# Kernel optimization log

Hardware: AMD Instinct MI355X
Metric: run time of the kernel (lower is better)

Reference implementation:

```python
import jax, jax.numpy as jnp
import numpy as np

EMBED_DIM = 1024
NUM_HEADS = 16
HEAD_DIM = EMBED_DIM // NUM_HEADS
B, T = 2, 2048


def setup_inputs() -> dict:
    key = jax.random.key(0)
    ks = jax.random.split(key, 5)
    s_in = 1.0 / np.sqrt(EMBED_DIM)
    return {
        "x": jax.random.normal(ks[0], (B, T, EMBED_DIM), dtype=jnp.float32),
        "qkv_w": jax.random.uniform(ks[1], (3 * EMBED_DIM, EMBED_DIM), jnp.float32, -s_in, s_in),
        "qkv_b": jax.random.uniform(ks[2], (3 * EMBED_DIM,), jnp.float32, -s_in, s_in),
        "out_w": jax.random.uniform(ks[3], (EMBED_DIM, EMBED_DIM), jnp.float32, -s_in, s_in),
        "out_b": jax.random.uniform(ks[4], (EMBED_DIM,), jnp.float32, -s_in, s_in),
    }


def reference(x, qkv_w, qkv_b, out_w, out_b):
    b, t, d = x.shape
    scale = HEAD_DIM ** -0.5
    # fused qkv projection: (B, T, 3D)
    qkv = jnp.einsum("btd,ed->bte", x, qkv_w) + qkv_b
    qkv = qkv.reshape(b, t, 3, NUM_HEADS, HEAD_DIM)
    q, k, v = jnp.moveaxis(qkv, 2, 0)  # each (B, T, H, Dh)
    # scores: (B, H, T, T)
    scores = jnp.einsum("bqhd,bkhd->bhqk", q, k) * scale
    attn = jax.nn.softmax(scores, axis=-1)
    # attention output: (B, T, H, Dh) -> (B, T, D)
    ctx = jnp.einsum("bhqk,bkhd->bqhd", attn, v).reshape(b, t, d)
    return jnp.einsum("btd,ed->bte", ctx, out_w) + out_b
```

## Files before the change

### kernel.cpp

```cpp
#include <hip/hip_runtime.h>

typedef __bf16 bf16;
typedef __bf16 bf16x4 __attribute__((ext_vector_type(4)));
typedef __bf16 bf16x8 __attribute__((ext_vector_type(8)));
typedef float f32x4 __attribute__((ext_vector_type(4)));

#define MFMA16(a, b, c) __builtin_amdgcn_mfma_f32_16x16x32_bf16(a, b, c, 0, 0, 0)

__device__ __forceinline__ void lds_load16(void* lds, const void* g) {
  __builtin_amdgcn_global_load_lds(
      (const __attribute__((address_space(1))) unsigned int*)g,
      (__attribute__((address_space(3))) unsigned int*)lds, 16, 0, 0);
}

__global__ void cvt3(const float* __restrict__ x, const float* __restrict__ qw,
                     const float* __restrict__ ow, bf16* __restrict__ xb,
                     bf16* __restrict__ qwb, bf16* __restrict__ owb) {
  const int i = blockIdx.x * blockDim.x + threadIdx.x;
  const float* src;
  bf16* dst;
  int k;
  if (i < 1048576) {
    src = x; dst = xb; k = i;
  } else if (i < 1048576 + 786432) {
    src = qw; dst = qwb; k = i - 1048576;
  } else {
    src = ow; dst = owb; k = i - (1048576 + 786432);
  }
  const float4 v = ((const float4*)src)[k];
  bf16x4 o;
  o[0] = (bf16)v.x; o[1] = (bf16)v.y; o[2] = (bf16)v.z; o[3] = (bf16)v.w;
  ((bf16x4*)dst)[k] = o;
}

template <int MODE>
__global__ __launch_bounds__(256, 2) void gemm_bt(
    const bf16* __restrict__ A, const bf16* __restrict__ B,
    const float* __restrict__ bias, float* __restrict__ Cf,
    bf16* __restrict__ Qb, bf16* __restrict__ Kb, bf16* __restrict__ VT,
    int N, int K) {
  __shared__ bf16 As[128][64];
  __shared__ bf16 Bs[128][64];
  const int tid = threadIdx.x;
  const int w = tid >> 6, lane = tid & 63;
  const int l15 = lane & 15, quad = lane >> 4;
  const int lr = lane >> 3;
  const int lc = (lane & 7) * 8;
  const int bn = blockIdx.x, bm = blockIdx.y;
  const int wm = (w >> 1) * 64, wn = (w & 1) * 64;

  const bf16* Abase = A + (size_t)(bm * 128) * K;
  const bf16* Bbase = B + (size_t)(bn * 128) * K;

  f32x4 acc[4][4] = {};

  for (int k0 = 0; k0 < K; k0 += 64) {
#pragma unroll
    for (int c = 0; c < 4; ++c) {
      const int row = w * 32 + c * 8;
      lds_load16(&As[row][0], Abase + (size_t)(row + lr) * K + k0 + lc);
      lds_load16(&Bs[row][0], Bbase + (size_t)(row + lr) * K + k0 + lc);
    }
    __syncthreads();
#pragma unroll
    for (int kk = 0; kk < 64; kk += 32) {
      bf16x8 am[4], bnf[4];
#pragma unroll
      for (int i = 0; i < 4; ++i)
        am[i] = *(const bf16x8*)&As[wm + i * 16 + l15][kk + quad * 8];
#pragma unroll
      for (int j = 0; j < 4; ++j)
        bnf[j] = *(const bf16x8*)&Bs[wn + j * 16 + l15][kk + quad * 8];
#pragma unroll
      for (int i = 0; i < 4; ++i)
#pragma unroll
        for (int j = 0; j < 4; ++j)
          acc[i][j] = MFMA16(am[i], bnf[j], acc[i][j]);
    }
    __syncthreads();
  }

#pragma unroll
  for (int j = 0; j < 4; ++j) {
    const int gcol = bn * 128 + wn + j * 16 + l15;
    const float bv = bias[gcol];
#pragma unroll
    for (int i = 0; i < 4; ++i) {
      const int t0 = bm * 128 + wm + i * 16 + quad * 4;
      if (MODE == 0) {
#pragma unroll
        for (int r = 0; r < 4; ++r)
          Cf[(size_t)(t0 + r) * N + gcol] = acc[i][j][r] + bv;
      } else if (gcol < 1024) {
#pragma unroll
        for (int r = 0; r < 4; ++r)
          Qb[(size_t)(t0 + r) * 1024 + gcol] =
              (bf16)((acc[i][j][r] + bv) * 0.125f);
      } else if (gcol < 2048) {
#pragma unroll
        for (int r = 0; r < 4; ++r)
          Kb[(size_t)(t0 + r) * 1024 + (gcol - 1024)] = (bf16)(acc[i][j][r] + bv);
      } else {
        const int b = t0 >> 11, t = t0 & 2047;
        const int hh = (gcol >> 6) & 15, dh = gcol & 63;
        bf16x4 pv;
#pragma unroll
        for (int r = 0; r < 4; ++r) pv[r] = (bf16)(acc[i][j][r] + bv);
        *(bf16x4*)&VT[(size_t)((b * 16 + hh) * 64 + dh) * 2048 + t] = pv;
      }
    }
  }
}

__global__ __launch_bounds__(256, 2) void attn(const bf16* __restrict__ Qb,
                                               const bf16* __restrict__ Kb,
                                               const bf16* __restrict__ VT,
                                               bf16* __restrict__ CTX) {
  __shared__ bf16 Ks[64][72];
  __shared__ bf16 Vs[64][72];
  __shared__ bf16 Ps[128][72];
  const int tid = threadIdx.x, w = tid >> 6, lane = tid & 63;
  const int l15 = lane & 15, quad = lane >> 4;
  const int blk = blockIdx.x;
  const int qt = blk & 15, h = (blk >> 4) & 15, b = blk >> 8;
  const int q0 = qt * 128;

  const bf16* kbase = Kb + (size_t)(b * 2048) * 1024 + h * 64;
  const bf16* vbase = VT + (size_t)((b * 16 + h) * 64) * 2048;

  const bf16* qrow0 =
      Qb + (size_t)(b * 2048 + q0 + w * 32 + l15) * 1024 + h * 64;
  const bf16* qrow1 = qrow0 + (size_t)16 * 1024;
  const bf16x8 bq0a = *(const bf16x8*)&qrow0[quad * 8];
  const bf16x8 bq0b = *(const bf16x8*)&qrow0[32 + quad * 8];
  const bf16x8 bq1a = *(const bf16x8*)&qrow1[quad * 8];
  const bf16x8 bq1b = *(const bf16x8*)&qrow1[32 + quad * 8];

  const int r0 = tid >> 3, col0 = (tid & 7) << 3;
  bf16x8 kreg0 = *(const bf16x8*)&kbase[(size_t)r0 * 1024 + col0];
  bf16x8 kreg1 = *(const bf16x8*)&kbase[(size_t)(r0 + 32) * 1024 + col0];
  bf16x8 vreg0 = *(const bf16x8*)&vbase[(size_t)r0 * 2048 + col0];
  bf16x8 vreg1 = *(const bf16x8*)&vbase[(size_t)(r0 + 32) * 2048 + col0];

  float m_run[2] = {-1e30f, -1e30f}, l_run[2] = {0.f, 0.f};
  f32x4 o[2][4] = {};

  for (int kt = 0; kt < 2048; kt += 64) {
    *(bf16x8*)&Ks[r0][col0] = kreg0;
    *(bf16x8*)&Ks[r0 + 32][col0] = kreg1;
    *(bf16x8*)&Vs[r0][col0] = vreg0;
    *(bf16x8*)&Vs[r0 + 32][col0] = vreg1;
    __syncthreads();

    if (kt < 2048 - 64) {
      const int nt = kt + 64;
      kreg0 = *(const bf16x8*)&kbase[(size_t)(nt + r0) * 1024 + col0];
      kreg1 = *(const bf16x8*)&kbase[(size_t)(nt + r0 + 32) * 1024 + col0];
      vreg0 = *(const bf16x8*)&vbase[(size_t)r0 * 2048 + nt + col0];
      vreg1 = *(const bf16x8*)&vbase[(size_t)(r0 + 32) * 2048 + nt + col0];
    }

    f32x4 s[2][4] = {};
#pragma unroll
    for (int kk = 0; kk < 64; kk += 32) {
#pragma unroll
      for (int j = 0; j < 4; ++j) {
        const bf16x8 ak = *(const bf16x8*)&Ks[j * 16 + l15][kk + quad * 8];
        s[0][j] = MFMA16(ak, kk ? bq0b : bq0a, s[0][j]);
        s[1][j] = MFMA16(ak, kk ? bq1b : bq1a, s[1][j]);
      }
    }

#pragma unroll
    for (int i = 0; i < 2; ++i) {
      float pm = s[i][0][0];
#pragma unroll
      for (int j = 0; j < 4; ++j)
#pragma unroll
        for (int r = 0; r < 4; ++r) pm = fmaxf(pm, s[i][j][r]);
      pm = fmaxf(pm, __shfl_xor(pm, 16));
      pm = fmaxf(pm, __shfl_xor(pm, 32));
      const float mnew = fmaxf(m_run[i], pm);
      const float alpha = __expf(m_run[i] - mnew);
      float sum = 0.f;
#pragma unroll
      for (int j = 0; j < 4; ++j)
#pragma unroll
        for (int r = 0; r < 4; ++r) {
          const float p = __expf(s[i][j][r] - mnew);
          s[i][j][r] = p;
          sum += p;
        }
      sum += __shfl_xor(sum, 16);
      sum += __shfl_xor(sum, 32);
      l_run[i] = l_run[i] * alpha + sum;
      m_run[i] = mnew;
#pragma unroll
      for (int j = 0; j < 4; ++j) {
#pragma unroll
        for (int r = 0; r < 4; ++r) o[i][j][r] *= alpha;
        bf16x4 pk;
#pragma unroll
        for (int r = 0; r < 4; ++r) pk[r] = (bf16)s[i][j][r];
        *(bf16x4*)&Ps[w * 32 + i * 16 + l15][j * 16 + quad * 4] = pk;
      }
    }

#pragma unroll
    for (int kk = 0; kk < 64; kk += 32) {
      const bf16x8 bp0 = *(const bf16x8*)&Ps[w * 32 + l15][kk + quad * 8];
      const bf16x8 bp1 = *(const bf16x8*)&Ps[w * 32 + 16 + l15][kk + quad * 8];
#pragma unroll
      for (int j = 0; j < 4; ++j) {
        const bf16x8 av = *(const bf16x8*)&Vs[j * 16 + l15][kk + quad * 8];
        o[0][j] = MFMA16(av, bp0, o[0][j]);
        o[1][j] = MFMA16(av, bp1, o[1][j]);
      }
    }
    __syncthreads();
  }

#pragma unroll
  for (int i = 0; i < 2; ++i) {
    const float inv = 1.f / l_run[i];
    bf16* crow =
        CTX + (size_t)(b * 2048 + q0 + w * 32 + i * 16 + l15) * 1024 + h * 64;
#pragma unroll
    for (int j = 0; j < 4; ++j) {
      bf16x4 ov;
#pragma unroll
      for (int r = 0; r < 4; ++r) ov[r] = (bf16)(o[i][j][r] * inv);
      *(bf16x4*)&crow[j * 16 + quad * 4] = ov;
    }
  }
}

extern "C" void kernel_launch(void* const* d_in, const int* in_sizes, int n_in,
                              void* d_out, int out_size, void* d_ws,
                              size_t ws_size, hipStream_t stream) {
  const float* x = (const float*)d_in[0];
  const float* qkv_w = (const float*)d_in[1];
  const float* qkv_b = (const float*)d_in[2];
  const float* out_w = (const float*)d_in[3];
  const float* out_b = (const float*)d_in[4];
  float* out = (float*)d_out;

  bf16* xb = (bf16*)d_ws;
  bf16* wqkv = xb + (size_t)4096 * 1024;
  bf16* wout = wqkv + (size_t)3072 * 1024;
  bf16* qb = wout + (size_t)1024 * 1024;
  bf16* kb = qb + (size_t)4096 * 1024;
  bf16* vt = kb + (size_t)4096 * 1024;
  bf16* ctx = vt + (size_t)4096 * 1024;

  cvt3<<<2097152 / 256, 256, 0, stream>>>(x, qkv_w, out_w, xb, wqkv, wout);

  gemm_bt<1><<<dim3(24, 32), 256, 0, stream>>>(xb, wqkv, qkv_b, nullptr, qb,
                                               kb, vt, 3072, 1024);
  attn<<<512, 256, 0, stream>>>(qb, kb, vt, ctx);
  gemm_bt<0><<<dim3(8, 32), 256, 0, stream>>>(ctx, wout, out_b, out, nullptr,
                                              nullptr, nullptr, 1024, 1024);
}
```

Baseline: 208.5 us.

## Load K and V fragments directly from global into registers, drop LDS staging

The attention kernel no longer stages K and V tiles through shared memory. Each wave loads its MFMA operand fragments straight from global memory (relying on L1/L2 reuse across the 4 waves), which removes the LDS writes, LDS reads and both block-wide barriers per key tile. The cost is that each wave redundantly fetches the full K/V tile from cache, and the register-prefetch pipelining is lost, so global load latency is exposed before the MFMAs unless the compiler hoists loads.

Result: slower. 279.7 us (+34.2%).

```diff
diff --git a/kernel.cpp b/kernel.cpp
--- a/kernel.cpp
+++ b/kernel.cpp
@@ -116,17 +116,12 @@
                                                const bf16* __restrict__ Kb,
                                                const bf16* __restrict__ VT,
                                                bf16* __restrict__ CTX) {
-  __shared__ bf16 Ks[64][72];
-  __shared__ bf16 Vs[64][72];
   __shared__ bf16 Ps[128][72];
   const int tid = threadIdx.x, w = tid >> 6, lane = tid & 63;
   const int l15 = lane & 15, quad = lane >> 4;
   const int blk = blockIdx.x;
   const int qt = blk & 15, h = (blk >> 4) & 15, b = blk >> 8;
   const int q0 = qt * 128;
-
-  const bf16* kbase = Kb + (size_t)(b * 2048) * 1024 + h * 64;
-  const bf16* vbase = VT + (size_t)((b * 16 + h) * 64) * 2048;
 
   const bf16* qrow0 =
       Qb + (size_t)(b * 2048 + q0 + w * 32 + l15) * 1024 + h * 64;
@@ -136,40 +131,38 @@
   const bf16x8 bq1a = *(const bf16x8*)&qrow1[quad * 8];
   const bf16x8 bq1b = *(const bf16x8*)&qrow1[32 + quad * 8];
 
-  const int r0 = tid >> 3, col0 = (tid & 7) << 3;
-  bf16x8 kreg0 = *(const bf16x8*)&kbase[(size_t)r0 * 1024 + col0];
-  bf16x8 kreg1 = *(const bf16x8*)&kbase[(size_t)(r0 + 32) * 1024 + col0];
-  bf16x8 vreg0 = *(const bf16x8*)&vbase[(size_t)r0 * 2048 + col0];
-  bf16x8 vreg1 = *(const bf16x8*)&vbase[(size_t)(r0 + 32) * 2048 + col0];
+  const bf16* krow = Kb + (size_t)(b * 2048 + l15) * 1024 + h * 64 + quad * 8;
+  const bf16* vrow =
+      VT + (size_t)((b * 16 + h) * 64 + l15) * 2048 + quad * 8;
 
   float m_run[2] = {-1e30f, -1e30f}, l_run[2] = {0.f, 0.f};
   f32x4 o[2][4] = {};
 
   for (int kt = 0; kt < 2048; kt += 64) {
-    *(bf16x8*)&Ks[r0][col0] = kreg0;
-    *(bf16x8*)&Ks[r0 + 32][col0] = kreg1;
-    *(bf16x8*)&Vs[r0][col0] = vreg0;
-    *(bf16x8*)&Vs[r0 + 32][col0] = vreg1;
-    __syncthreads();
-
-    if (kt < 2048 - 64) {
-      const int nt = kt + 64;
-      kreg0 = *(const bf16x8*)&kbase[(size_t)(nt + r0) * 1024 + col0];
-      kreg1 = *(const bf16x8*)&kbase[(size_t)(nt + r0 + 32) * 1024 + col0];
-      vreg0 = *(const bf16x8*)&vbase[(size_t)r0 * 2048 + nt + col0];
-      vreg1 = *(const bf16x8*)&vbase[(size_t)(r0 + 32) * 2048 + nt + col0];
-    }
+    bf16x8 kf[2][4];
+#pragma unroll
+    for (int j = 0; j < 4; ++j)
+#pragma unroll
+      for (int k2 = 0; k2 < 2; ++k2)
+        kf[k2][j] =
+            *(const bf16x8*)&krow[(size_t)(kt + j * 16) * 1024 + k2 * 32];
 
     f32x4 s[2][4] = {};
 #pragma unroll
-    for (int kk = 0; kk < 64; kk += 32) {
+    for (int k2 = 0; k2 < 2; ++k2)
 #pragma unroll
       for (int j = 0; j < 4; ++j) {
-        const bf16x8 ak = *(const bf16x8*)&Ks[j * 16 + l15][kk + quad * 8];
-        s[0][j] = MFMA16(ak, kk ? bq0b : bq0a, s[0][j]);
-        s[1][j] = MFMA16(ak, kk ? bq1b : bq1a, s[1][j]);
-      }
-    }
+        s[0][j] = MFMA16(kf[k2][j], k2 ? bq0b : bq0a, s[0][j]);
+        s[1][j] = MFMA16(kf[k2][j], k2 ? bq1b : bq1a, s[1][j]);
+      }
+
+    bf16x8 vf[2][4];
+#pragma unroll
+    for (int j = 0; j < 4; ++j)
+#pragma unroll
+      for (int k2 = 0; k2 < 2; ++k2)
+        vf[k2][j] =
+            *(const bf16x8*)&vrow[(size_t)(j * 16) * 2048 + kt + k2 * 32];
 
 #pragma unroll
     for (int i = 0; i < 2; ++i) {
@@ -207,17 +200,17 @@
     }
 
 #pragma unroll
-    for (int kk = 0; kk < 64; kk += 32) {
-      const bf16x8 bp0 = *(const bf16x8*)&Ps[w * 32 + l15][kk + quad * 8];
-      const bf16x8 bp1 = *(const bf16x8*)&Ps[w * 32 + 16 + l15][kk + quad * 8];
+    for (int k2 = 0; k2 < 2; ++k2) {
+      const bf16x8 bp0 =
+          *(const bf16x8*)&Ps[w * 32 + l15][k2 * 32 + quad * 8];
+      const bf16x8 bp1 =
+          *(const bf16x8*)&Ps[w * 32 + 16 + l15][k2 * 32 + quad * 8];
 #pragma unroll
       for (int j = 0; j < 4; ++j) {
-        const bf16x8 av = *(const bf16x8*)&Vs[j * 16 + l15][kk + quad * 8];
-        o[0][j] = MFMA16(av, bp0, o[0][j]);
-        o[1][j] = MFMA16(av, bp1, o[1][j]);
-      }
-    }
-    __syncthreads();
+        o[0][j] = MFMA16(vf[k2][j], bp0, o[0][j]);
+        o[1][j] = MFMA16(vf[k2][j], bp1, o[1][j]);
+      }
+    }
   }
 
 #pragma unroll
```
